# Kernel optimization log

Hardware: AMD Instinct MI355X
Metric: run time of the kernel (lower is better)

The kernel has to match this reference:

```python
import jax, jax.numpy as jnp
import numpy as np


def _gru(x, Wih, Whh, bih, bhh):
    # PyTorch GRU cell math, batch=1: x [S, IN], Wih [3H, IN], Whh [3H, H]
    H = Whh.shape[1]
    def step(h, xt):
        gi = Wih @ xt + bih
        gh = Whh @ h + bhh
        i_r, i_z, i_n = jnp.split(gi, 3)
        h_r, h_z, h_n = jnp.split(gh, 3)
        r = jax.nn.sigmoid(i_r + h_r)
        z = jax.nn.sigmoid(i_z + h_z)
        n = jnp.tanh(i_n + r * h_n)
        hn = (1.0 - z) * n + z * h
        return hn, hn
    _, hs = jax.lax.scan(step, jnp.zeros((H,), x.dtype), x)
    return hs  # [S, H]


def setup_inputs() -> dict:
    key = jax.random.key(0)
    ks = jax.random.split(key, 18)
    LOC, TIM, UID = 100000, 48, 5000
    DL, DT, DU, H = 256, 32, 64, 256
    SEQ, NH, TOT, TGT = 2048, 4096, 16384, 1024
    IN = DL + DT  # 288
    s = 0.02
    return {
        "loc": jax.random.randint(ks[0], (SEQ,), 0, LOC),
        "tim": jax.random.randint(ks[1], (SEQ,), 0, TIM),
        "history_loc": jax.random.randint(ks[2], (TOT,), 0, LOC),
        "history_tim": jax.random.randint(ks[3], (TOT,), 0, TIM),
        "history_count": jnp.full((NH,), TOT // NH, dtype=jnp.int32),
        "uid": jax.random.randint(ks[4], (1,), 0, UID),
        "target_len": TGT,
        "emb_loc": jax.random.normal(ks[5], (LOC, DL), jnp.float32) * s,
        "emb_tim": jax.random.normal(ks[6], (TIM, DT), jnp.float32) * s,
        "emb_uid": jax.random.normal(ks[7], (UID, DU), jnp.float32) * s,
        "W_attn": jax.random.normal(ks[8], (2 * H, IN), jnp.float32) * s,
        "b_attn": jnp.zeros((2 * H,), jnp.float32),
        "Wih_f": jax.random.normal(ks[9], (3 * H, IN), jnp.float32) * s,
        "Whh_f": jax.random.normal(ks[10], (3 * H, H), jnp.float32) * s,
        "bih_f": jnp.zeros((3 * H,), jnp.float32),
        "bhh_f": jnp.zeros((3 * H,), jnp.float32),
        "Wih_b": jax.random.normal(ks[11], (3 * H, IN), jnp.float32) * s,
        "Whh_b": jax.random.normal(ks[12], (3 * H, H), jnp.float32) * s,
        "bih_b": jnp.zeros((3 * H,), jnp.float32),
        "bhh_b": jnp.zeros((3 * H,), jnp.float32),
        "Wf": jax.random.normal(ks[13], (LOC, 4 * H + DU), jnp.float32) * s,
        "bf": jnp.zeros((LOC,), jnp.float32),
    }


def reference(loc, tim, history_loc, history_tim, history_count, uid, target_len,
              emb_loc, emb_tim, emb_uid, W_attn, b_attn,
              Wih_f, Whh_f, bih_f, bhh_f, Wih_b, Whh_b, bih_b, bhh_b, Wf, bf):
    counts = np.asarray(jax.device_get(history_count))  # static ragged structure
    n = counts.shape[0]
    seg = jnp.asarray(np.repeat(np.arange(n), counts))
    offs = jnp.asarray(np.concatenate([[0], np.cumsum(counts)[:-1]]))

    # current trajectory embedding [S, IN] (dropout is identity in eval)
    x = jnp.concatenate([emb_loc[loc], emb_tim[tim]], axis=1)

    # ragged segment mean of history loc embeddings; first tim embedding per group
    le = emb_loc[history_loc]  # [TOT, DL]
    loc_mean = jax.ops.segment_sum(le, seg, num_segments=n) / counts.astype(le.dtype)[:, None]
    tim_first = emb_tim[history_tim][offs]  # [n, DT]
    history = jnp.tanh(jnp.concatenate([loc_mean, tim_first], axis=1) @ W_attn.T + b_attn)  # [n, 2H]

    # bidirectional GRU, batch 1
    hf = _gru(x, Wih_f, Whh_f, bih_f, bhh_f)
    hb = _gru(x[::-1], Wih_b, Whh_b, bih_b, bhh_b)[::-1]
    out_state = jnp.concatenate([hf, hb], axis=1)  # [S, 2H]

    q = out_state[-target_len:]                      # [T, 2H]
    attn = jax.nn.softmax(q @ history.T, axis=1)     # dot-product attention
    context = attn @ history                         # [T, 2H]

    uid_emb = jnp.broadcast_to(emb_uid[uid], (target_len, emb_uid.shape[1]))
    out = jnp.concatenate([q, context, uid_emb], axis=1)  # [T, 4H+DU]
    return jax.nn.log_softmax(out @ Wf.T + bf, axis=1)    # [T, LOC]
```

## Files before the change

### kernel.cpp

```cpp
#include <hip/hip_runtime.h>
#include <hip/hip_bf16.h>
#include <stdint.h>

typedef unsigned int uint;
typedef unsigned short ushort;

#define SEQ   2048
#define TGT   1024
#define HDIM  256
#define IN3   288
#define G3    768
#define NHIST 4096
#define DL    256
#define DT    32
#define DU    64
#define NLOC  100000
#define DOUT  1088

typedef _Float16 half2_t __attribute__((ext_vector_type(2)));
typedef short short8 __attribute__((ext_vector_type(8)));
typedef float floatx4 __attribute__((ext_vector_type(4)));
typedef float float4v __attribute__((ext_vector_type(4)));
typedef ushort ushort8v __attribute__((ext_vector_type(8)));

__device__ __forceinline__ ushort f2bf(float f) {
  uint u = __builtin_bit_cast(uint, f);
  u += 0x7FFFu + ((u >> 16) & 1u);
  return (ushort)(u >> 16);
}
__device__ __forceinline__ float fdot2u(uint a, uint b, float c) {
  return __builtin_amdgcn_fdot2(__builtin_bit_cast(half2_t, a),
                                __builtin_bit_cast(half2_t, b), c, false);
}

__global__ void k_pack_whh(const float* __restrict__ whf, const float* __restrict__ whb,
                           uint* __restrict__ wpack) {
  int idx = blockIdx.x * 256 + threadIdx.x;
  int dir = idx / 98304;
  int rem = idx - dir * 98304;
  int k2 = rem / 768;
  int row = rem - k2 * 768;
  const float* W = dir ? whb : whf;
  float w0 = W[row * 256 + 2 * k2];
  float w1 = W[row * 256 + 2 * k2 + 1];
  half2_t h = { (_Float16)w0, (_Float16)w1 };
  wpack[idx] = __builtin_bit_cast(uint, h);
}

__global__ void k_embed_x(const int* __restrict__ loc, const int* __restrict__ tim,
                          const float* __restrict__ emb_loc, const float* __restrict__ emb_tim,
                          ushort* __restrict__ xb) {
  int t = blockIdx.x;
  int tid = threadIdx.x;
  int l = loc[t], m = tim[t];
  if (tid < 256) xb[(size_t)t * IN3 + tid] = f2bf(emb_loc[(size_t)l * DL + tid]);
  if (tid < 32)  xb[(size_t)t * IN3 + 256 + tid] = f2bf(emb_tim[m * DT + tid]);
}

__global__ void k_scan(const int* __restrict__ counts, int* __restrict__ offs) {
  __shared__ int sd[1024];
  int tid = threadIdx.x;
  int base = tid * 4;
  int c0 = counts[base], c1 = counts[base + 1], c2 = counts[base + 2], c3 = counts[base + 3];
  int tot = c0 + c1 + c2 + c3;
  sd[tid] = tot;
  __syncthreads();
  int val = tot;
  for (int off = 1; off < 1024; off <<= 1) {
    int v = (tid >= off) ? sd[tid - off] : 0;
    __syncthreads();
    val += v;
    sd[tid] = val;
    __syncthreads();
  }
  int excl = val - tot;
  offs[base] = excl;
  offs[base + 1] = excl + c0;
  offs[base + 2] = excl + c0 + c1;
  offs[base + 3] = excl + c0 + c1 + c2;
}

__global__ void k_hin(const int* __restrict__ hloc, const int* __restrict__ htim,
                      const int* __restrict__ counts, const int* __restrict__ offs,
                      const float* __restrict__ emb_loc, const float* __restrict__ emb_tim,
                      ushort* __restrict__ hin) {
  int i = blockIdx.x;
  int tid = threadIdx.x;
  int off = offs[i], cnt = counts[i];
  float4v s = {0.f, 0.f, 0.f, 0.f};
  for (int e = 0; e < cnt; ++e) {
    int l = hloc[off + e];
    const float4v* row = (const float4v*)(emb_loc + (size_t)l * DL);
    s += row[tid];
  }
  float inv = 1.f / (float)cnt;
  size_t b = (size_t)i * IN3 + tid * 4;
  hin[b + 0] = f2bf(s[0] * inv);
  hin[b + 1] = f2bf(s[1] * inv);
  hin[b + 2] = f2bf(s[2] * inv);
  hin[b + 3] = f2bf(s[3] * inv);
  if (tid < 32) {
    int ht = htim[off];
    hin[(size_t)i * IN3 + 256 + tid] = f2bf(emb_tim[ht * DT + tid]);
  }
}

template<bool BF32, int ACT>
__global__ __launch_bounds__(256, 2)
void k_gemm(const ushort* __restrict__ A, const void* __restrict__ Bv,
            const float* __restrict__ bias, float* __restrict__ C,
            int M, int N, int K) {
  __shared__ __align__(16) ushort As[128 * 40];
  __shared__ __align__(16) ushort Bs[128 * 40];
  const int tid = threadIdx.x;
  const int m0 = blockIdx.x * 128;
  const int n0 = blockIdx.y * 128;
  const int wave = tid >> 6, lane = tid & 63;
  const int wm = (wave & 1) << 6, wn = (wave >> 1) << 6;
  const int r16 = lane & 15, kq = lane >> 4;
  floatx4 acc[4][4];
  for (int i = 0; i < 4; i++)
    for (int j = 0; j < 4; j++)
      acc[i][j] = (floatx4){0.f, 0.f, 0.f, 0.f};
  const int srow = tid >> 1;
  const int scol = (tid & 1) << 4;
  const bool bok = (n0 + srow) < N;
  for (int k0 = 0; k0 < K; k0 += 32) {
    const ushort* ap = A + (size_t)(m0 + srow) * K + k0 + scol;
    uint4 a0 = *(const uint4*)ap;
    uint4 a1 = *(const uint4*)(ap + 8);
    *(uint4*)&As[srow * 40 + scol] = a0;
    *(uint4*)&As[srow * 40 + scol + 8] = a1;
    if (BF32) {
      const float* bp = (const float*)Bv + (size_t)(n0 + srow) * K + k0 + scol;
      float4v b0 = {0,0,0,0}, b1 = {0,0,0,0}, b2 = {0,0,0,0}, b3 = {0,0,0,0};
      if (bok) {
        b0 = ((const float4v*)bp)[0];
        b1 = ((const float4v*)bp)[1];
        b2 = ((const float4v*)bp)[2];
        b3 = ((const float4v*)bp)[3];
      }
      ushort8v v0, v1;
      for (int j = 0; j < 4; j++) {
        v0[j] = f2bf(b0[j]); v0[4 + j] = f2bf(b1[j]);
        v1[j] = f2bf(b2[j]); v1[4 + j] = f2bf(b3[j]);
      }
      *(ushort8v*)&Bs[srow * 40 + scol] = v0;
      *(ushort8v*)&Bs[srow * 40 + scol + 8] = v1;
    } else {
      const ushort* bp = (const ushort*)Bv + (size_t)(n0 + srow) * K + k0 + scol;
      uint4 z = {0u, 0u, 0u, 0u};
      uint4 b0 = bok ? *(const uint4*)bp : z;
      uint4 b1 = bok ? *(const uint4*)(bp + 8) : z;
      *(uint4*)&Bs[srow * 40 + scol] = b0;
      *(uint4*)&Bs[srow * 40 + scol + 8] = b1;
    }
    __syncthreads();
    short8 af[4], bfr[4];
    #pragma unroll
    for (int i = 0; i < 4; i++) af[i] = *(const short8*)&As[(wm + i * 16 + r16) * 40 + kq * 8];
    #pragma unroll
    for (int i = 0; i < 4; i++) bfr[i] = *(const short8*)&Bs[(wn + i * 16 + r16) * 40 + kq * 8];
    #pragma unroll
    for (int i = 0; i < 4; i++)
      #pragma unroll
      for (int j = 0; j < 4; j++)
        acc[i][j] = __builtin_amdgcn_mfma_f32_16x16x32_bf16(af[i], bfr[j], acc[i][j], 0, 0, 0);
    __syncthreads();
  }
  #pragma unroll
  for (int j = 0; j < 4; j++) {
    int col = n0 + wn + j * 16 + r16;
    if (col >= N) continue;
    float bv = bias ? bias[col] : 0.f;
    #pragma unroll
    for (int i = 0; i < 4; i++) {
      #pragma unroll
      for (int r = 0; r < 4; r++) {
        int row = m0 + wm + i * 16 + kq * 4 + r;
        float v = acc[i][j][r] + bv;
        if (ACT == 1) v = tanhf(v);
        C[(size_t)row * N + col] = v;
      }
    }
  }
}

__global__ void k_hist_cast(const float* __restrict__ Hf, ushort* __restrict__ Hb,
                            ushort* __restrict__ HTb) {
  __shared__ float tle[64][65];
  int i0 = blockIdx.x * 64;
  int j0 = blockIdx.y * 64;
  int tid = threadIdx.x;
  #pragma unroll
  for (int rep = 0; rep < 16; ++rep) {
    int idx = rep * 256 + tid;
    int r = idx >> 6, c = idx & 63;
    float v = Hf[(size_t)(i0 + r) * 512 + j0 + c];
    tle[r][c] = v;
    Hb[(size_t)(i0 + r) * 512 + j0 + c] = f2bf(v);
  }
  __syncthreads();
  #pragma unroll
  for (int rep = 0; rep < 16; ++rep) {
    int idx = rep * 256 + tid;
    int r = idx >> 6, c = idx & 63;
    HTb[(size_t)(j0 + r) * 4096 + i0 + c] = f2bf(tle[c][r]);
  }
}

__global__ __launch_bounds__(512, 2)
void k_gru(const float* __restrict__ gi_f, const float* __restrict__ gi_b,
           const uint* __restrict__ wpack,
           const float* __restrict__ bhh_f, const float* __restrict__ bhh_b,
           ushort* __restrict__ qb) {
  const int dir = blockIdx.x;
  const int tid = threadIdx.x;
  const int dim = tid & 255;
  const int half = tid >> 8;
  const int lane = tid & 63;
  const float* gi = dir ? gi_b : gi_f;
  const float* bhh = dir ? bhh_b : bhh_f;
  const uint* wp = wpack + dir * (128 * 768) + (half * 64) * 768;
  uint wr[64], wz[64], wn_[64];
  #pragma unroll
  for (int j = 0; j < 64; ++j) {
    wr[j]  = wp[j * 768 + dim];
    wz[j]  = wp[j * 768 + 256 + dim];
    wn_[j] = wp[j * 768 + 512 + dim];
  }
  const float b_r = bhh[dim], b_z = bhh[256 + dim], b_n = bhh[512 + dim];
  __shared__ _Float16 hbuf[2][256];
  __shared__ float pbuf[2][3][256];
  uint h2 = 0u;
  float h_cur = 0.f;
  int t0 = dir ? 2047 : 0;
  float gi0 = gi[t0 * 768 + dim];
  float gi1 = gi[t0 * 768 + 256 + dim];
  float gi2 = gi[t0 * 768 + 512 + dim];
  for (int s = 0; s < 2048; ++s) {
    int tn = dir ? (2046 - s) : (s + 1);
    tn = tn < 0 ? 0 : (tn > 2047 ? 2047 : tn);
    float ngi0 = gi[tn * 768 + dim];
    float ngi1 = gi[tn * 768 + 256 + dim];
    float ngi2 = gi[tn * 768 + 512 + dim];
    float ar0 = 0.f, ar1 = 0.f, az0 = 0.f, az1 = 0.f, an0 = 0.f, an1 = 0.f;
    #pragma unroll
    for (int j = 0; j < 64; j += 2) {
      uint s0 = (uint)__builtin_amdgcn_readlane((int)h2, j);
      ar0 = fdot2u(wr[j], s0, ar0);
      az0 = fdot2u(wz[j], s0, az0);
      an0 = fdot2u(wn_[j], s0, an0);
      uint s1 = (uint)__builtin_amdgcn_readlane((int)h2, j + 1);
      ar1 = fdot2u(wr[j + 1], s1, ar1);
      az1 = fdot2u(wz[j + 1], s1, az1);
      an1 = fdot2u(wn_[j + 1], s1, an1);
    }
    pbuf[half][0][dim] = ar0 + ar1;
    pbuf[half][1][dim] = az0 + az1;
    pbuf[half][2][dim] = an0 + an1;
    __syncthreads();
    if (half == 0) {
      float gr = pbuf[0][0][dim] + pbuf[1][0][dim] + b_r + gi0;
      float gz = pbuf[0][1][dim] + pbuf[1][1][dim] + b_z + gi1;
      float gn = pbuf[0][2][dim] + pbuf[1][2][dim] + b_n;
      float r = 1.f / (1.f + __expf(-gr));
      float z = 1.f / (1.f + __expf(-gz));
      float x = gi2 + r * gn;
      float nn = 1.f - 2.f / (__expf(2.f * x) + 1.f);
      h_cur = (1.f - z) * nn + z * h_cur;
      hbuf[s & 1][dim] = (_Float16)h_cur;
      if (dir == 0) {
        if (s >= 1024) qb[(size_t)(s - 1024) * 512 + dim] = f2bf(h_cur);
      } else {
        if (s < 1024) qb[(size_t)(1023 - s) * 512 + 256 + dim] = f2bf(h_cur);
      }
    }
    __syncthreads();
    h2 = ((const uint*)hbuf[s & 1])[half * 64 + lane];
    gi0 = ngi0; gi1 = ngi1; gi2 = ngi2;
  }
}

__global__ void k_softmax(const float* __restrict__ S, ushort* __restrict__ P) {
  int m = blockIdx.x;
  int tid = threadIdx.x;
  const float* row = S + (size_t)m * 4096;
  float ev[16];
  float mx = -3.0e38f;
  #pragma unroll
  for (int i = 0; i < 16; i++) {
    float x = row[tid + i * 256];
    ev[i] = x;
    mx = fmaxf(mx, x);
  }
  #pragma unroll
  for (int o = 32; o > 0; o >>= 1) mx = fmaxf(mx, __shfl_xor(mx, o));
  __shared__ float red[4];
  __shared__ float red2[4];
  int w = tid >> 6, l = tid & 63;
  if (l == 0) red[w] = mx;
  __syncthreads();
  mx = fmaxf(fmaxf(red[0], red[1]), fmaxf(red[2], red[3]));
  float sm = 0.f;
  #pragma unroll
  for (int i = 0; i < 16; i++) {
    ev[i] = __expf(ev[i] - mx);
    sm += ev[i];
  }
  #pragma unroll
  for (int o = 32; o > 0; o >>= 1) sm += __shfl_xor(sm, o);
  if (l == 0) red2[w] = sm;
  __syncthreads();
  sm = red2[0] + red2[1] + red2[2] + red2[3];
  float inv = 1.f / sm;
  #pragma unroll
  for (int i = 0; i < 16; i++)
    P[(size_t)m * 4096 + tid + i * 256] = f2bf(ev[i] * inv);
}

__global__ void k_assemble(const ushort* __restrict__ qb, const float* __restrict__ ctx,
                           const float* __restrict__ emb_uid, const int* __restrict__ uid,
                           ushort* __restrict__ ob) {
  int m = blockIdx.x, tid = threadIdx.x;
  int u = uid[0];
  for (int c = tid; c < DOUT; c += 256) {
    ushort v;
    if (c < 512) v = qb[(size_t)m * 512 + c];
    else if (c < 1024) v = f2bf(ctx[(size_t)m * 512 + (c - 512)]);
    else v = f2bf(emb_uid[(size_t)u * DU + (c - 1024)]);
    ob[(size_t)m * DOUT + c] = v;
  }
}

__global__ void k_lse(const float* __restrict__ logits, float* __restrict__ lse) {
  int m = blockIdx.x, tid = threadIdx.x;
  const float* row = logits + (size_t)m * NLOC;
  float mx = -3.0e38f, sm = 0.f;
  for (int c = tid; c < NLOC; c += 256) {
    float x = row[c];
    float nm = fmaxf(mx, x);
    sm = sm * __expf(mx - nm) + __expf(x - nm);
    mx = nm;
  }
  #pragma unroll
  for (int o = 32; o > 0; o >>= 1) {
    float omx = __shfl_xor(mx, o);
    float osm = __shfl_xor(sm, o);
    float nm = fmaxf(mx, omx);
    sm = sm * __expf(mx - nm) + osm * __expf(omx - nm);
    mx = nm;
  }
  __shared__ float smx[4], ssm[4];
  int w = tid >> 6;
  if ((tid & 63) == 0) { smx[w] = mx; ssm[w] = sm; }
  __syncthreads();
  if (tid == 0) {
    float M = fmaxf(fmaxf(smx[0], smx[1]), fmaxf(smx[2], smx[3]));
    float S = ssm[0] * __expf(smx[0] - M) + ssm[1] * __expf(smx[1] - M)
            + ssm[2] * __expf(smx[2] - M) + ssm[3] * __expf(smx[3] - M);
    lse[m] = M + logf(S);
  }
}

__global__ void k_sub(float* __restrict__ out, const float* __restrict__ lse) {
  int i = blockIdx.x * 256 + threadIdx.x;
  if (i >= TGT * (NLOC / 4)) return;
  int rowq = i / (NLOC / 4);
  float4v v = ((float4v*)out)[i];
  float l = lse[rowq];
  v[0] -= l; v[1] -= l; v[2] -= l; v[3] -= l;
  ((float4v*)out)[i] = v;
}

extern "C" void kernel_launch(void* const* d_in, const int* in_sizes, int n_in,
                              void* d_out, int out_size, void* d_ws, size_t ws_size,
                              hipStream_t stream) {
  const int*   loc     = (const int*)d_in[0];
  const int*   tim     = (const int*)d_in[1];
  const int*   hloc    = (const int*)d_in[2];
  const int*   htim    = (const int*)d_in[3];
  const int*   hcnt    = (const int*)d_in[4];
  const int*   uid     = (const int*)d_in[5];
  const float* emb_loc = (const float*)d_in[7];
  const float* emb_tim = (const float*)d_in[8];
  const float* emb_uid = (const float*)d_in[9];
  const float* W_attn  = (const float*)d_in[10];
  const float* b_attn  = (const float*)d_in[11];
  const float* Wih_f   = (const float*)d_in[12];
  const float* Whh_f   = (const float*)d_in[13];
  const float* bih_f   = (const float*)d_in[14];
  const float* bhh_f   = (const float*)d_in[15];
  const float* Wih_b   = (const float*)d_in[16];
  const float* Whh_b   = (const float*)d_in[17];
  const float* bih_b   = (const float*)d_in[18];
  const float* bhh_b   = (const float*)d_in[19];
  const float* Wf      = (const float*)d_in[20];
  const float* bfv     = (const float*)d_in[21];
  float* out = (float*)d_out;

  char* w = (char*)d_ws;
  size_t o = 0;
  auto take = [&](size_t bytes) -> void* {
    o = (o + 511) & ~(size_t)511;
    void* p = w + o;
    o += bytes;
    return p;
  };
  int*    offs   = (int*)take(4096 * 4);
  ushort* xb     = (ushort*)take((size_t)SEQ * IN3 * 2);
  ushort* hin    = (ushort*)take((size_t)NHIST * IN3 * 2);
  float*  gi_f   = (float*)take((size_t)SEQ * G3 * 4);
  float*  gi_b   = (float*)take((size_t)SEQ * G3 * 4);
  uint*   wpack  = (uint*)take((size_t)2 * 128 * 768 * 4);
  float*  hist   = (float*)take((size_t)NHIST * 512 * 4);
  ushort* histb  = (ushort*)take((size_t)NHIST * 512 * 2);
  ushort* histTb = (ushort*)take((size_t)512 * NHIST * 2);
  ushort* qb     = (ushort*)take((size_t)TGT * 512 * 2);
  float*  scores = (float*)take((size_t)TGT * NHIST * 4);
  ushort* attnb  = (ushort*)take((size_t)TGT * NHIST * 2);
  float*  ctx    = (float*)take((size_t)TGT * 512 * 4);
  ushort* ob     = (ushort*)take((size_t)TGT * DOUT * 2);
  float*  lsebuf = (float*)take((size_t)TGT * 4);

  k_pack_whh<<<768, 256, 0, stream>>>(Whh_f, Whh_b, wpack);
  k_embed_x<<<SEQ, 256, 0, stream>>>(loc, tim, emb_loc, emb_tim, xb);
  k_scan<<<1, 1024, 0, stream>>>(hcnt, offs);
  k_hin<<<NHIST, 64, 0, stream>>>(hloc, htim, hcnt, offs, emb_loc, emb_tim, hin);

  k_gemm<true, 0><<<dim3(16, 6), 256, 0, stream>>>(xb, (const void*)Wih_f, bih_f, gi_f, SEQ, G3, IN3);
  k_gemm<true, 0><<<dim3(16, 6), 256, 0, stream>>>(xb, (const void*)Wih_b, bih_b, gi_b, SEQ, G3, IN3);

  k_gemm<true, 1><<<dim3(32, 4), 256, 0, stream>>>(hin, (const void*)W_attn, b_attn, hist, NHIST, 512, IN3);
  k_hist_cast<<<dim3(64, 8), 256, 0, stream>>>(hist, histb, histTb);

  k_gru<<<2, 512, 0, stream>>>(gi_f, gi_b, wpack, bhh_f, bhh_b, qb);

  k_gemm<false, 0><<<dim3(8, 32), 256, 0, stream>>>(qb, (const void*)histb, nullptr, scores, TGT, NHIST, 512);
  k_softmax<<<TGT, 256, 0, stream>>>(scores, attnb);
  k_gemm<false, 0><<<dim3(8, 4), 256, 0, stream>>>(attnb, (const void*)histTb, nullptr, ctx, TGT, 512, NHIST);

  k_assemble<<<TGT, 256, 0, stream>>>(qb, ctx, emb_uid, uid, ob);
  k_gemm<true, 0><<<dim3(8, 782), 256, 0, stream>>>(ob, (const void*)Wf, bfv, out, TGT, NLOC, DOUT);

  k_lse<<<TGT, 256, 0, stream>>>(out, lsebuf);
  k_sub<<<(TGT * (NLOC / 4) + 255) / 256, 256, 0, stream>>>(out, lsebuf);
}
```

Baseline: 4.606 ms.

## Compute GRU recurrent matvec with MFMA instead of fdot2 readlane loops

The recurrent W_hh·h product in the GRU kernel now runs on MFMA 16x16x32 f16 instructions. Each of 8 waves keeps 96 rows of packed weights in registers as A fragments. The hidden state is fed as the B operand, with only one column nonzero (lanes read a zero buffer otherwise). The goal is to remove the long serial chain of readlane plus dot2 ops and the two-half partial-sum reduction on the sequential critical path. In exchange, most of the MFMA work is wasted on zero columns, and per-step latency now depends on MFMA issue and dependency latency.

```diff
diff --git a/kernel.cpp b/kernel.cpp
--- a/kernel.cpp
+++ b/kernel.cpp
@@ -17,34 +17,37 @@
 #define NLOC  100000
 #define DOUT  1088
 
-typedef _Float16 half2_t __attribute__((ext_vector_type(2)));
 typedef short short8 __attribute__((ext_vector_type(8)));
 typedef float floatx4 __attribute__((ext_vector_type(4)));
 typedef float float4v __attribute__((ext_vector_type(4)));
 typedef ushort ushort8v __attribute__((ext_vector_type(8)));
+typedef _Float16 half8v __attribute__((ext_vector_type(8)));
 
 __device__ __forceinline__ ushort f2bf(float f) {
   uint u = __builtin_bit_cast(uint, f);
   u += 0x7FFFu + ((u >> 16) & 1u);
   return (ushort)(u >> 16);
 }
-__device__ __forceinline__ float fdot2u(uint a, uint b, float c) {
-  return __builtin_amdgcn_fdot2(__builtin_bit_cast(half2_t, a),
-                                __builtin_bit_cast(half2_t, b), c, false);
-}
 
 __global__ void k_pack_whh(const float* __restrict__ whf, const float* __restrict__ whb,
-                           uint* __restrict__ wpack) {
+                           uint4* __restrict__ wpack) {
   int idx = blockIdx.x * 256 + threadIdx.x;
-  int dir = idx / 98304;
-  int rem = idx - dir * 98304;
-  int k2 = rem / 768;
-  int row = rem - k2 * 768;
+  int dir = idx / 24576;
+  int r = idx - dir * 24576;
+  int wave = r / 3072;
+  int r2 = r - wave * 3072;
+  int rt = r2 / 512;
+  int r3 = r2 - rt * 512;
+  int kt = r3 / 64;
+  int lane = r3 - kt * 64;
+  int row = wave * 96 + rt * 16 + (lane & 15);
+  int kb = kt * 32 + (lane >> 4) * 8;
   const float* W = dir ? whb : whf;
-  float w0 = W[row * 256 + 2 * k2];
-  float w1 = W[row * 256 + 2 * k2 + 1];
-  half2_t h = { (_Float16)w0, (_Float16)w1 };
-  wpack[idx] = __builtin_bit_cast(uint, h);
+  const float* src = W + (size_t)row * 256 + kb;
+  half8v h;
+  #pragma unroll
+  for (int j = 0; j < 8; ++j) h[j] = (_Float16)src[j];
+  wpack[idx] = __builtin_bit_cast(uint4, h);
 }
 
 __global__ void k_embed_x(const int* __restrict__ loc, const int* __restrict__ tim,
@@ -211,65 +214,84 @@
 
 __global__ __launch_bounds__(512, 2)
 void k_gru(const float* __restrict__ gi_f, const float* __restrict__ gi_b,
-           const uint* __restrict__ wpack,
+           const uint4* __restrict__ wpack,
            const float* __restrict__ bhh_f, const float* __restrict__ bhh_b,
            ushort* __restrict__ qb) {
   const int dir = blockIdx.x;
   const int tid = threadIdx.x;
-  const int dim = tid & 255;
-  const int half = tid >> 8;
-  const int lane = tid & 63;
+  const int wave = tid >> 6, lane = tid & 63;
   const float* gi = dir ? gi_b : gi_f;
   const float* bhh = dir ? bhh_b : bhh_f;
-  const uint* wp = wpack + dir * (128 * 768) + (half * 64) * 768;
-  uint wr[64], wz[64], wn_[64];
-  #pragma unroll
-  for (int j = 0; j < 64; ++j) {
-    wr[j]  = wp[j * 768 + dim];
-    wz[j]  = wp[j * 768 + 256 + dim];
-    wn_[j] = wp[j * 768 + 512 + dim];
-  }
-  const float b_r = bhh[dim], b_z = bhh[256 + dim], b_n = bhh[512 + dim];
-  __shared__ _Float16 hbuf[2][256];
-  __shared__ float pbuf[2][3][256];
-  uint h2 = 0u;
+
+  __shared__ __align__(16) _Float16 hbuf[256];
+  __shared__ __align__(16) _Float16 zbuf[256];
+  __shared__ __align__(16) float ghs[768];
+
+  half8v afr[6][8];
+  {
+    const uint4* wp = wpack + (size_t)dir * 24576 + wave * 3072 + lane;
+    #pragma unroll
+    for (int rt = 0; rt < 6; ++rt)
+      #pragma unroll
+      for (int kt = 0; kt < 8; ++kt)
+        afr[rt][kt] = __builtin_bit_cast(half8v, wp[rt * 512 + kt * 64]);
+  }
+  if (tid < 256) { hbuf[tid] = (_Float16)0.f; zbuf[tid] = (_Float16)0.f; }
+
+  const _Float16* bsrc = ((lane & 15) == 0) ? (hbuf + (lane >> 4) * 8) : zbuf;
+  const int gw_row = wave * 96 + (lane >> 4) * 4;
+  const bool gw_ok = ((lane & 15) == 0);
+
+  const int dim = tid;
+  float b_r = 0.f, b_z = 0.f, b_n = 0.f;
+  float gi0 = 0.f, gi1 = 0.f, gi2 = 0.f;
+  if (tid < 256) {
+    b_r = bhh[dim]; b_z = bhh[256 + dim]; b_n = bhh[512 + dim];
+    int t0 = dir ? 2047 : 0;
+    gi0 = gi[(size_t)t0 * 768 + dim];
+    gi1 = gi[(size_t)t0 * 768 + 256 + dim];
+    gi2 = gi[(size_t)t0 * 768 + 512 + dim];
+  }
   float h_cur = 0.f;
-  int t0 = dir ? 2047 : 0;
-  float gi0 = gi[t0 * 768 + dim];
-  float gi1 = gi[t0 * 768 + 256 + dim];
-  float gi2 = gi[t0 * 768 + 512 + dim];
+  __syncthreads();
+
   for (int s = 0; s < 2048; ++s) {
     int tn = dir ? (2046 - s) : (s + 1);
     tn = tn < 0 ? 0 : (tn > 2047 ? 2047 : tn);
-    float ngi0 = gi[tn * 768 + dim];
-    float ngi1 = gi[tn * 768 + 256 + dim];
-    float ngi2 = gi[tn * 768 + 512 + dim];
-    float ar0 = 0.f, ar1 = 0.f, az0 = 0.f, az1 = 0.f, an0 = 0.f, an1 = 0.f;
-    #pragma unroll
-    for (int j = 0; j < 64; j += 2) {
-      uint s0 = (uint)__builtin_amdgcn_readlane((int)h2, j);
-      ar0 = fdot2u(wr[j], s0, ar0);
-      az0 = fdot2u(wz[j], s0, az0);
-      an0 = fdot2u(wn_[j], s0, an0);
-      uint s1 = (uint)__builtin_amdgcn_readlane((int)h2, j + 1);
-      ar1 = fdot2u(wr[j + 1], s1, ar1);
-      az1 = fdot2u(wz[j + 1], s1, az1);
-      an1 = fdot2u(wn_[j + 1], s1, an1);
-    }
-    pbuf[half][0][dim] = ar0 + ar1;
-    pbuf[half][1][dim] = az0 + az1;
-    pbuf[half][2][dim] = an0 + an1;
-    __syncthreads();
-    if (half == 0) {
-      float gr = pbuf[0][0][dim] + pbuf[1][0][dim] + b_r + gi0;
-      float gz = pbuf[0][1][dim] + pbuf[1][1][dim] + b_z + gi1;
-      float gn = pbuf[0][2][dim] + pbuf[1][2][dim] + b_n;
+    float ngi0 = 0.f, ngi1 = 0.f, ngi2 = 0.f;
+    if (tid < 256) {
+      ngi0 = gi[(size_t)tn * 768 + dim];
+      ngi1 = gi[(size_t)tn * 768 + 256 + dim];
+      ngi2 = gi[(size_t)tn * 768 + 512 + dim];
+    }
+
+    floatx4 acc[6];
+    #pragma unroll
+    for (int rt = 0; rt < 6; ++rt) acc[rt] = (floatx4){0.f, 0.f, 0.f, 0.f};
+    #pragma unroll
+    for (int kt = 0; kt < 8; ++kt) {
+      half8v b = *(const half8v*)(bsrc + kt * 32);
+      #pragma unroll
+      for (int rt = 0; rt < 6; ++rt)
+        acc[rt] = __builtin_amdgcn_mfma_f32_16x16x32_f16(afr[rt][kt], b, acc[rt], 0, 0, 0);
+    }
+    if (gw_ok) {
+      #pragma unroll
+      for (int rt = 0; rt < 6; ++rt)
+        *(floatx4*)&ghs[gw_row + rt * 16] = acc[rt];
+    }
+    __syncthreads();
+
+    if (tid < 256) {
+      float gr = ghs[dim] + b_r + gi0;
+      float gz = ghs[256 + dim] + b_z + gi1;
+      float gn = ghs[512 + dim] + b_n;
       float r = 1.f / (1.f + __expf(-gr));
       float z = 1.f / (1.f + __expf(-gz));
       float x = gi2 + r * gn;
       float nn = 1.f - 2.f / (__expf(2.f * x) + 1.f);
       h_cur = (1.f - z) * nn + z * h_cur;
-      hbuf[s & 1][dim] = (_Float16)h_cur;
+      hbuf[dim] = (_Float16)h_cur;
       if (dir == 0) {
         if (s >= 1024) qb[(size_t)(s - 1024) * 512 + dim] = f2bf(h_cur);
       } else {
@@ -277,7 +299,6 @@
       }
     }
     __syncthreads();
-    h2 = ((const uint*)hbuf[s & 1])[half * 64 + lane];
     gi0 = ngi0; gi1 = ngi1; gi2 = ngi2;
   }
 }
@@ -412,7 +433,7 @@
   ushort* hin    = (ushort*)take((size_t)NHIST * IN3 * 2);
   float*  gi_f   = (float*)take((size_t)SEQ * G3 * 4);
   float*  gi_b   = (float*)take((size_t)SEQ * G3 * 4);
-  uint*   wpack  = (uint*)take((size_t)2 * 128 * 768 * 4);
+  uint4*  wpack  = (uint4*)take((size_t)49152 * sizeof(uint4));
   float*  hist   = (float*)take((size_t)NHIST * 512 * 4);
   ushort* histb  = (ushort*)take((size_t)NHIST * 512 * 2);
   ushort* histTb = (ushort*)take((size_t)512 * NHIST * 2);
@@ -423,7 +444,7 @@
   ushort* ob     = (ushort*)take((size_t)TGT * DOUT * 2);
   float*  lsebuf = (float*)take((size_t)TGT * 4);
 
-  k_pack_whh<<<768, 256, 0, stream>>>(Whh_f, Whh_b, wpack);
+  k_pack_whh<<<192, 256, 0, stream>>>(Whh_f, Whh_b, wpack);
   k_embed_x<<<SEQ, 256, 0, stream>>>(loc, tim, emb_loc, emb_tim, xb);
   k_scan<<<1, 1024, 0, stream>>>(hcnt, offs);
   k_hin<<<NHIST, 64, 0, stream>>>(hloc, htim, hcnt, offs, emb_loc, emb_tim, hin);
```

New measurement: 4.355 ms. 1.06x faster.
